# Kernel tuning notes

Measured on AMD Instinct MI355X. Metric: run time of the kernel, lower is better.

The kernel has to match this reference:

```python
import jax, jax.numpy as jnp
import numpy as np

B, T, C = 128, 512, 512
EPS = 1e-5


def setup_inputs() -> dict:
    key = jax.random.key(0)
    ks = jax.random.split(key, 12)
    s_tri = 1.0 / np.sqrt(T)   # rough torch Linear init scale (per-row fan-in varies; fixed for simplicity)
    s_fc1 = 1.0 / np.sqrt(C)
    s_fc2 = 1.0 / np.sqrt(2 * C)
    return {
        "inputs": jax.random.normal(ks[0], (B, T, C), dtype=jnp.float32),
        "ln1_w": jnp.ones((T, C), jnp.float32),
        "ln1_b": jnp.zeros((T, C), jnp.float32),
        "ln2_w": jnp.ones((T, C), jnp.float32),
        "ln2_b": jnp.zeros((T, C), jnp.float32),
        # Row s of triu_W corresponds to nn.Linear(s+1, 1); entries j> s are masked in reference().
        "triu_W": jax.random.uniform(ks[1], (T, T), jnp.float32, -s_tri, s_tri),
        "triu_b": jax.random.uniform(ks[2], (T,), jnp.float32, -s_tri, s_tri),
        "fc1_W": jax.random.uniform(ks[3], (2 * C, C), jnp.float32, -s_fc1, s_fc1),
        "fc1_b": jax.random.uniform(ks[4], (2 * C,), jnp.float32, -s_fc1, s_fc1),
        "fc2_W": jax.random.uniform(ks[5], (C, 2 * C), jnp.float32, -s_fc2, s_fc2),
        "fc2_b": jax.random.uniform(ks[6], (C,), jnp.float32, -s_fc2, s_fc2),
    }


def _layernorm_2d(x, w, b):
    # torch nn.LayerNorm((T, C)): normalize jointly over the last TWO dims.
    mu = jnp.mean(x, axis=(-2, -1), keepdims=True)
    var = jnp.var(x, axis=(-2, -1), keepdims=True)
    return (x - mu) * jax.lax.rsqrt(var + EPS) * w + b


def reference(inputs, ln1_w, ln1_b, ln2_w, ln2_b, triu_W, triu_b, fc1_W, fc1_b, fc2_W, fc2_b):
    x = _layernorm_2d(inputs, ln1_w, ln1_b)                       # [B,T,C]
    # TriU time mixer on x.mT ([B,C,T]): out[..., s] = sum_{t<=s} W[s,t]*x[..., t] + b[s]
    Wm = jnp.tril(triu_W)                                          # causal mask
    xm = jnp.einsum('btc,st->bsc', x, Wm) + triu_b[None, :, None]  # [B,T,C] (already back-transposed)
    x2 = _layernorm_2d(xm + inputs, ln2_w, ln2_b)                  # [B,T,C]
    h = jax.nn.gelu(jnp.einsum('btc,hc->bth', x2, fc1_W) + fc1_b, approximate=False)
    y = jnp.einsum('bth,ch->btc', h, fc2_W) + fc2_b
    return x2 + y
```

## Files before the change

### kernel.cpp

```cpp
#include <hip/hip_runtime.h>
#include <cstdint>

typedef unsigned short u16;
typedef __attribute__((ext_vector_type(8))) short s16x8;
typedef __attribute__((ext_vector_type(4))) float f32x4;
typedef __attribute__((ext_vector_type(8))) unsigned short u16x8;
typedef __attribute__((ext_vector_type(4))) unsigned short u16x4;

#define B_ 128
#define T_ 512
#define C_ 512
#define TC 262144

static __device__ __forceinline__ float bf2f(u16 u) {
  union { unsigned int i; float f; } v; v.i = ((unsigned int)u) << 16; return v.f;
}
static __device__ __forceinline__ u16 f2bf(float f) {
  union { float fv; unsigned int i; } v; v.fv = f;
  unsigned int r = (v.i + 0x7FFFu + ((v.i >> 16) & 1u)) >> 16;
  return (u16)r;
}

static __device__ __forceinline__ float gelu_fast(float x) {
  float x2 = x * x;
  float arg = 1.5957691216057308f * x * fmaf(0.044715f, x2, 1.0f);
  return x / (1.0f + __expf(-arg));
}

#define GLD16(gp, lp) __builtin_amdgcn_global_load_lds( \
    (const __attribute__((address_space(1))) void*)(gp), \
    (__attribute__((address_space(3))) void*)(lp), 16, 0, 0)


__global__ __launch_bounds__(256)
void reduce_stats_kernel(const float* __restrict__ X, float2* __restrict__ partials) {
  const int b = blockIdx.y, blk = blockIdx.x, tid = threadIdx.x;
  const float* p = X + (size_t)b * TC + (size_t)blk * 2048 + (size_t)tid * 8;
  f32x4 v0 = *(const f32x4*)p;
  f32x4 v1 = *(const f32x4*)(p + 4);
  float s = 0.f, q = 0.f;
#pragma unroll
  for (int i = 0; i < 4; ++i) { s += v0[i] + v1[i]; q += v0[i] * v0[i] + v1[i] * v1[i]; }
  for (int o = 32; o; o >>= 1) { s += __shfl_down(s, o); q += __shfl_down(q, o); }
  __shared__ float ss[4], qq[4];
  if ((tid & 63) == 0) { ss[tid >> 6] = s; qq[tid >> 6] = q; }
  __syncthreads();
  if (tid == 0)
    partials[(size_t)b * 128 + blk] =
        make_float2(ss[0] + ss[1] + ss[2] + ss[3], qq[0] + qq[1] + qq[2] + qq[3]);
}

__global__ __launch_bounds__(128)
void finalize_stats_kernel(const float2* __restrict__ partials, float2* __restrict__ stats) {
  const int b = blockIdx.x, tid = threadIdx.x;
  float2 v = partials[(size_t)b * 128 + tid];
  float s = v.x, q = v.y;
  for (int o = 32; o; o >>= 1) { s += __shfl_down(s, o); q += __shfl_down(q, o); }
  __shared__ float ss[2], qq[2];
  if ((tid & 63) == 0) { ss[tid >> 6] = s; qq[tid >> 6] = q; }
  __syncthreads();
  if (tid == 0) {
    float sm = ss[0] + ss[1], sq = qq[0] + qq[1];
    float mean = sm * (1.f / (float)TC);
    float var = sq * (1.f / (float)TC) - mean * mean;
    stats[b] = make_float2(mean, rsqrtf(var + 1e-5f));
  }
}

__global__ __launch_bounds__(64)
void finalize_stats4_kernel(const float2* __restrict__ partials, float2* __restrict__ stats) {
  const int b = blockIdx.x, tid = threadIdx.x;
  float s = 0.f, q = 0.f;
  if (tid < 4) { float2 v = partials[(size_t)b * 4 + tid]; s = v.x; q = v.y; }
  for (int o = 2; o; o >>= 1) { s += __shfl_down(s, o); q += __shfl_down(q, o); }
  if (tid == 0) {
    float mean = s * (1.f / (float)TC);
    float var = q * (1.f / (float)TC) - mean * mean;
    stats[b] = make_float2(mean, rsqrtf(var + 1e-5f));
  }
}


__global__ __launch_bounds__(256)
void ln1_transpose_kernel(const float* __restrict__ X, const float* __restrict__ W,
                          const float* __restrict__ Bv, const float2* __restrict__ stats,
                          u16* __restrict__ xT) {
  const int b = blockIdx.z;
  const int t0 = blockIdx.y * 64, c0 = blockIdx.x * 64;
  const float2 st = stats[b];
  const float mu = st.x, rs = st.y;
  __shared__ u16 tile[64][72];
  const int tid = threadIdx.x;
  const int rr = tid >> 4;
  const int cc = (tid & 15) * 4;
#pragma unroll
  for (int i = 0; i < 4; ++i) {
    const int lt = i * 16 + rr;
    const size_t wi = (size_t)(t0 + lt) * C_ + c0 + cc;
    f32x4 x = *(const f32x4*)(X + (size_t)b * TC + wi);
    f32x4 w = *(const f32x4*)(W + wi);
    f32x4 bb = *(const f32x4*)(Bv + wi);
#pragma unroll
    for (int j = 0; j < 4; ++j)
      tile[lt][cc + j] = f2bf((x[j] - mu) * rs * w[j] + bb[j]);
  }
  __syncthreads();
  const int c = tid >> 2;
  const int tg = (tid & 3) * 16;
  u16 buf[16];
#pragma unroll
  for (int i = 0; i < 16; ++i) buf[i] = tile[tg + i][c];
  const size_t o = (size_t)b * TC + (size_t)(c0 + c) * T_ + t0 + tg;
  u16x8 o0, o1;
#pragma unroll
  for (int i = 0; i < 8; ++i) { o0[i] = buf[i]; o1[i] = buf[8 + i]; }
  *(u16x8*)(xT + o) = o0;
  *(u16x8*)(xT + o + 8) = o1;
}


__global__ __launch_bounds__(256)
void ln2_apply_kernel(const u16* __restrict__ S, const float* __restrict__ W,
                      const float* __restrict__ Bv, const float2* __restrict__ stats,
                      u16* __restrict__ x2) {
  const size_t i = ((size_t)blockIdx.x * 256 + threadIdx.x) * 8;
  const int b = (int)(i >> 18);
  const size_t r = i & (size_t)(TC - 1);
  const float2 st = stats[b];
  const float mu = st.x, rs = st.y;
  u16x8 sv = *(const u16x8*)(S + i);
  f32x4 w0 = *(const f32x4*)(W + r);
  f32x4 w1 = *(const f32x4*)(W + r + 4);
  f32x4 b0 = *(const f32x4*)(Bv + r);
  f32x4 b1 = *(const f32x4*)(Bv + r + 4);
  u16x8 o;
#pragma unroll
  for (int j = 0; j < 4; ++j) {
    o[j]     = f2bf((bf2f(sv[j])     - mu) * rs * w0[j] + b0[j]);
    o[4 + j] = f2bf((bf2f(sv[4 + j]) - mu) * rs * w1[j] + b1[j]);
  }
  *(u16x8*)(x2 + i) = o;
}


__global__ __launch_bounds__(256)
void cvt_bf16_kernel(const float* __restrict__ X, u16* __restrict__ Y) {
  const size_t i = ((size_t)blockIdx.x * 256 + threadIdx.x) * 4;
  f32x4 v = *(const f32x4*)(X + i);
  u16x4 o;
#pragma unroll
  for (int j = 0; j < 4; ++j) o[j] = f2bf(v[j]);
  *(u16x4*)(Y + i) = o;
}

__global__ __launch_bounds__(256)
void tril_bf16_kernel(const float* __restrict__ Wt, u16* __restrict__ Y) {
  const int i = blockIdx.x * 256 + threadIdx.x;
  const int s = i >> 9, t = i & 511;
  Y[i] = f2bf(t <= s ? Wt[i] : 0.f);
}


template <int MODE>
__global__ __launch_bounds__(512, 2)
void gemm_bt_kernel(const u16* __restrict__ A, const u16* __restrict__ Bm,
                    int K, int lda, int ldb,
                    void* __restrict__ Cp, int ldc,
                    const float* __restrict__ bias,
                    const void* __restrict__ res,
                    long long strideB, long long strideC,
                    float2* __restrict__ stat_part) {
  __shared__ u16 As[2][256 * 64];
  __shared__ u16 Bs[2][256 * 64];
  const int tid = threadIdx.x;

  const int nwg = gridDim.x;
  const int orig = blockIdx.x;
  const int swz = (orig & 7) * (nwg >> 3) + (orig >> 3);
  int bx, by, bz;
  if (MODE == 0) { bz = swz >> 2; by = (swz >> 1) & 1; bx = swz & 1; }
  else if (MODE == 1) { bz = 0; by = swz >> 2; bx = swz & 3; }
  else { bz = 0; by = swz >> 1; bx = swz & 1; }

  const u16* Bp = Bm + (size_t)bz * (size_t)strideB;
  const int m0 = by * 256, n0 = bx * 256;
  int kTiles = K >> 6;
  if (MODE == 0) { const int need = (by + 1) * 4; if (need < kTiles) kTiles = need; }

  const int lane = tid & 63;
  const int wave = tid >> 6;
  const int wm = (wave >> 2) * 128;
  const int wn = (wave & 3) * 64;
  const int lr = lane & 15;
  const int kg = lane >> 4;

  f32x4 acc[8][4];
  const f32x4 zero = {0.f, 0.f, 0.f, 0.f};
#pragma unroll
  for (int m = 0; m < 8; ++m)
#pragma unroll
    for (int n = 0; n < 4; ++n) acc[m][n] = zero;

  auto STAGE = [&](int buf, int kt) {
    const int k0 = kt << 6;
#pragma unroll
    for (int p = 0; p < 4; ++p) {
      const int q = p * 512 + tid;
      const int r = q >> 3;
      const int kcs = (q & 7) ^ (r & 7);
      GLD16(A + (size_t)(m0 + r) * lda + k0 + (kcs << 3), &As[buf][q * 8]);
    }
#pragma unroll
    for (int p = 0; p < 4; ++p) {
      const int q = p * 512 + tid;
      const int r = q >> 3;
      const int kcs = (q & 7) ^ (r & 7);
      GLD16(Bp + (size_t)(n0 + r) * ldb + k0 + (kcs << 3), &Bs[buf][q * 8]);
    }
  };

  STAGE(0, 0);
  int cur = 0;
  for (int kt = 0; kt < kTiles; ++kt) {
    __syncthreads();
    if (kt + 1 < kTiles) STAGE(cur ^ 1, kt + 1);
#pragma unroll
    for (int kk = 0; kk < 2; ++kk) {
      s16x8 af[8], bf4[4];
#pragma unroll
      for (int m = 0; m < 8; ++m) {
        const int row = wm + m * 16 + lr;
        const int ch = (kk * 4 + kg) ^ (row & 7);
        af[m] = *(const s16x8*)&As[cur][row * 64 + ch * 8];
      }
#pragma unroll
      for (int n = 0; n < 4; ++n) {
        const int row = wn + n * 16 + lr;
        const int ch = (kk * 4 + kg) ^ (row & 7);
        bf4[n] = *(const s16x8*)&Bs[cur][row * 64 + ch * 8];
      }
#pragma unroll
      for (int m = 0; m < 8; ++m)
#pragma unroll
        for (int n = 0; n < 4; ++n)
          acc[m][n] = __builtin_amdgcn_mfma_f32_16x16x32_bf16(af[m], bf4[n], acc[m][n], 0, 0, 0);
    }
    cur ^= 1;
  }

  if (MODE == 0) {
    u16* Cptr = (u16*)Cp + (size_t)bz * (size_t)strideC;
    const float* inp = (const float*)res + (size_t)bz * (size_t)strideC;
    float psum = 0.f, psq = 0.f;
#pragma unroll
    for (int m = 0; m < 8; ++m) {
      const int rb = m0 + wm + m * 16 + kg * 4;
#pragma unroll
      for (int n = 0; n < 4; ++n) {
        const int col = n0 + wn + n * 16 + lr;
#pragma unroll
        for (int j = 0; j < 4; ++j) {
          const size_t idx = (size_t)(rb + j) * ldc + col;
          float v = acc[m][n][j] + inp[idx] + bias[rb + j];
          psum += v; psq += v * v;
          Cptr[idx] = f2bf(v);
        }
      }
    }
    for (int o = 32; o; o >>= 1) { psum += __shfl_down(psum, o); psq += __shfl_down(psq, o); }
    __shared__ float rs_[8], rq_[8];
    if (lane == 0) { rs_[wave] = psum; rq_[wave] = psq; }
    __syncthreads();
    if (tid == 0) {
      float s = 0.f, q = 0.f;
#pragma unroll
      for (int w = 0; w < 8; ++w) { s += rs_[w]; q += rq_[w]; }
      stat_part[(size_t)bz * 4 + by * 2 + bx] = make_float2(s, q);
    }
  } else if (MODE == 1) {
    u16* Cptr = (u16*)Cp;
#pragma unroll
    for (int m = 0; m < 8; ++m) {
      const int rb = m0 + wm + m * 16 + kg * 4;
#pragma unroll
      for (int n = 0; n < 4; ++n) {
        const int col = n0 + wn + n * 16 + lr;
        const float bs = bias[col];
#pragma unroll
        for (int j = 0; j < 4; ++j) {
          float v = acc[m][n][j] + bs;
          Cptr[(size_t)(rb + j) * ldc + col] = f2bf(gelu_fast(v));
        }
      }
    }
  } else {
    float* Cptr = (float*)Cp;
    const u16* x2p = (const u16*)res;
#pragma unroll
    for (int m = 0; m < 8; ++m) {
      const int rb = m0 + wm + m * 16 + kg * 4;
#pragma unroll
      for (int n = 0; n < 4; ++n) {
        const int col = n0 + wn + n * 16 + lr;
        const float bs = bias[col];
#pragma unroll
        for (int j = 0; j < 4; ++j) {
          const size_t idx = (size_t)(rb + j) * ldc + col;
          Cptr[idx] = acc[m][n][j] + bs + bf2f(x2p[idx]);
        }
      }
    }
  }
}


extern "C" void kernel_launch(void* const* d_in, const int* in_sizes, int n_in,
                              void* d_out, int out_size, void* d_ws, size_t ws_size,
                              hipStream_t stream) {
  const float* inputs = (const float*)d_in[0];
  const float* ln1_w  = (const float*)d_in[1];
  const float* ln1_b  = (const float*)d_in[2];
  const float* ln2_w  = (const float*)d_in[3];
  const float* ln2_b  = (const float*)d_in[4];
  const float* triu_W = (const float*)d_in[5];
  const float* triu_b = (const float*)d_in[6];
  const float* fc1_W  = (const float*)d_in[7];
  const float* fc1_b  = (const float*)d_in[8];
  const float* fc2_W  = (const float*)d_in[9];
  const float* fc2_b  = (const float*)d_in[10];
  float* out = (float*)d_out;
  (void)in_sizes; (void)n_in; (void)out_size; (void)ws_size;

  char* ws = (char*)d_ws;
  size_t off = 0;
  auto carve = [&](size_t bytes) {
    char* p = ws + off;
    off += (bytes + 255) & ~(size_t)255;
    return p;
  };
  u16* s_bf = (u16*)carve((size_t)B_ * T_ * C_ * 2);
  u16* xT   = (u16*)carve((size_t)B_ * T_ * C_ * 2);
  u16* x2   = xT;
  u16* h    = (u16*)carve((size_t)B_ * T_ * 2 * C_ * 2);
  u16* wmb  = (u16*)carve((size_t)T_ * T_ * 2);
  u16* w1b  = (u16*)carve((size_t)2 * C_ * C_ * 2);
  u16* w2b  = (u16*)carve((size_t)C_ * 2 * C_ * 2);
  float2* partials  = (float2*)carve(128 * 128 * sizeof(float2));
  float2* partials2 = (float2*)carve(128 * 4 * sizeof(float2));
  float2* stats1 = (float2*)carve(128 * sizeof(float2));
  float2* stats2 = (float2*)carve(128 * sizeof(float2));

  reduce_stats_kernel<<<dim3(128, 128), 256, 0, stream>>>(inputs, partials);
  finalize_stats_kernel<<<128, 128, 0, stream>>>(partials, stats1);
  ln1_transpose_kernel<<<dim3(8, 8, 128), 256, 0, stream>>>(inputs, ln1_w, ln1_b, stats1, xT);
  tril_bf16_kernel<<<1024, 256, 0, stream>>>(triu_W, wmb);
  cvt_bf16_kernel<<<512, 256, 0, stream>>>(fc1_W, w1b);
  cvt_bf16_kernel<<<512, 256, 0, stream>>>(fc2_W, w2b);
  gemm_bt_kernel<0><<<512, 512, 0, stream>>>(
      wmb, xT, 512, 512, 512, s_bf, 512, triu_b, inputs, (long long)TC, (long long)TC, partials2);
  finalize_stats4_kernel<<<128, 64, 0, stream>>>(partials2, stats2);
  ln2_apply_kernel<<<16384, 256, 0, stream>>>(s_bf, ln2_w, ln2_b, stats2, x2);
  gemm_bt_kernel<1><<<1024, 512, 0, stream>>>(
      x2, w1b, 512, 512, 512, h, 1024, fc1_b, nullptr, 0, 0, nullptr);
  gemm_bt_kernel<2><<<512, 512, 0, stream>>>(
      h, w2b, 1024, 1024, 1024, out, 512, fc2_b, x2, 0, 0, nullptr);
}
```

Baseline: 404.5 us.

## Stage GEMM epilogues through swizzled LDS for coalesced vector global stores

All three GEMM epilogue modes now write accumulator fragments into the shared-memory buffer (XOR-swizzled to avoid bank conflicts), then re-read it row-wise so each thread issues wide 16-byte global loads and stores. Before, each lane wrote scattered 2- or 4-byte elements with strided residual reads. The aim is to cut uncoalesced global traffic in the epilogue. The cost is extra LDS round trips and barriers, and MODE 0 now rounds the accumulator to bf16 before adding the residual and bias, which slightly changes its numerics.

```diff
diff --git a/kernel.cpp b/kernel.cpp
--- a/kernel.cpp
+++ b/kernel.cpp
@@ -170,8 +170,10 @@
                     const void* __restrict__ res,
                     long long strideB, long long strideC,
                     float2* __restrict__ stat_part) {
-  __shared__ u16 As[2][256 * 64];
-  __shared__ u16 Bs[2][256 * 64];
+  __shared__ u16 smem[65536];
+  __shared__ float rs_[8], rq_[8];
+  u16* Asb = smem;
+  u16* Bsb = smem + 32768;
   const int tid = threadIdx.x;
 
   const int nwg = gridDim.x;
@@ -208,14 +210,14 @@
       const int q = p * 512 + tid;
       const int r = q >> 3;
       const int kcs = (q & 7) ^ (r & 7);
-      GLD16(A + (size_t)(m0 + r) * lda + k0 + (kcs << 3), &As[buf][q * 8]);
+      GLD16(A + (size_t)(m0 + r) * lda + k0 + (kcs << 3), &Asb[buf * 16384 + q * 8]);
     }
 #pragma unroll
     for (int p = 0; p < 4; ++p) {
       const int q = p * 512 + tid;
       const int r = q >> 3;
       const int kcs = (q & 7) ^ (r & 7);
-      GLD16(Bp + (size_t)(n0 + r) * ldb + k0 + (kcs << 3), &Bs[buf][q * 8]);
+      GLD16(Bp + (size_t)(n0 + r) * ldb + k0 + (kcs << 3), &Bsb[buf * 16384 + q * 8]);
     }
   };
 
@@ -231,13 +233,13 @@
       for (int m = 0; m < 8; ++m) {
         const int row = wm + m * 16 + lr;
         const int ch = (kk * 4 + kg) ^ (row & 7);
-        af[m] = *(const s16x8*)&As[cur][row * 64 + ch * 8];
+        af[m] = *(const s16x8*)&Asb[cur * 16384 + row * 64 + ch * 8];
       }
 #pragma unroll
       for (int n = 0; n < 4; ++n) {
         const int row = wn + n * 16 + lr;
         const int ch = (kk * 4 + kg) ^ (row & 7);
-        bf4[n] = *(const s16x8*)&Bs[cur][row * 64 + ch * 8];
+        bf4[n] = *(const s16x8*)&Bsb[cur * 16384 + row * 64 + ch * 8];
       }
 #pragma unroll
       for (int m = 0; m < 8; ++m)
@@ -247,28 +249,50 @@
     }
     cur ^= 1;
   }
+
+  __syncthreads();
+  char* ep = (char*)smem;
 
   if (MODE == 0) {
     u16* Cptr = (u16*)Cp + (size_t)bz * (size_t)strideC;
     const float* inp = (const float*)res + (size_t)bz * (size_t)strideC;
+#pragma unroll
+    for (int m = 0; m < 8; ++m)
+#pragma unroll
+      for (int n = 0; n < 4; ++n) {
+        const int col = wn + n * 16 + lr;
+#pragma unroll
+        for (int j = 0; j < 4; ++j) {
+          const int row = wm + m * 16 + kg * 4 + j;
+          const int byt = row * 512 + ((((col >> 3) ^ (row & 31)) << 4)) + (col & 7) * 2;
+          *(u16*)(ep + byt) = f2bf(acc[m][n][j]);
+        }
+      }
+    __syncthreads();
+    const int frow = tid >> 1;
+    const int fhalf = tid & 1;
+    const int grow = m0 + frow;
+    const float bs = bias[grow];
+    u16* Crow = Cptr + (size_t)grow * ldc + n0 + fhalf * 128;
+    const float* irow = inp + (size_t)grow * ldc + n0 + fhalf * 128;
     float psum = 0.f, psq = 0.f;
 #pragma unroll
-    for (int m = 0; m < 8; ++m) {
-      const int rb = m0 + wm + m * 16 + kg * 4;
-#pragma unroll
-      for (int n = 0; n < 4; ++n) {
-        const int col = n0 + wn + n * 16 + lr;
-#pragma unroll
-        for (int j = 0; j < 4; ++j) {
-          const size_t idx = (size_t)(rb + j) * ldc + col;
-          float v = acc[m][n][j] + inp[idx] + bias[rb + j];
-          psum += v; psq += v * v;
-          Cptr[idx] = f2bf(v);
-        }
-      }
-    }
-    for (int o = 32; o; o >>= 1) { psum += __shfl_down(psum, o); psq += __shfl_down(psq, o); }
-    __shared__ float rs_[8], rq_[8];
+    for (int c16 = 0; c16 < 16; ++c16) {
+      const int c = fhalf * 16 + c16;
+      u16x8 e = *(const u16x8*)(ep + frow * 512 + ((c ^ (frow & 31)) << 4));
+      f32x4 i0 = *(const f32x4*)(irow + c16 * 8);
+      f32x4 i1 = *(const f32x4*)(irow + c16 * 8 + 4);
+      u16x8 o;
+#pragma unroll
+      for (int k = 0; k < 4; ++k) {
+        float v0 = bf2f(e[k]) + i0[k] + bs;
+        float v1 = bf2f(e[4 + k]) + i1[k] + bs;
+        psum += v0 + v1; psq += v0 * v0 + v1 * v1;
+        o[k] = f2bf(v0); o[4 + k] = f2bf(v1);
+      }
+      *(u16x8*)(Crow + c16 * 8) = o;
+    }
+    for (int sh = 32; sh; sh >>= 1) { psum += __shfl_down(psum, sh); psq += __shfl_down(psq, sh); }
     if (lane == 0) { rs_[wave] = psum; rq_[wave] = psq; }
     __syncthreads();
     if (tid == 0) {
@@ -280,35 +304,67 @@
   } else if (MODE == 1) {
     u16* Cptr = (u16*)Cp;
 #pragma unroll
-    for (int m = 0; m < 8; ++m) {
-      const int rb = m0 + wm + m * 16 + kg * 4;
+    for (int m = 0; m < 8; ++m)
 #pragma unroll
       for (int n = 0; n < 4; ++n) {
-        const int col = n0 + wn + n * 16 + lr;
-        const float bs = bias[col];
+        const int coll = wn + n * 16 + lr;
+        const float bsn = bias[n0 + coll];
 #pragma unroll
         for (int j = 0; j < 4; ++j) {
-          float v = acc[m][n][j] + bs;
-          Cptr[(size_t)(rb + j) * ldc + col] = f2bf(gelu_fast(v));
+          const int row = wm + m * 16 + kg * 4 + j;
+          const int byt = row * 512 + ((((coll >> 3) ^ (row & 31)) << 4)) + (coll & 7) * 2;
+          *(u16*)(ep + byt) = f2bf(gelu_fast(acc[m][n][j] + bsn));
         }
       }
+    __syncthreads();
+    const int frow = tid >> 1;
+    const int fhalf = tid & 1;
+    const int grow = m0 + frow;
+    u16* Crow = Cptr + (size_t)grow * ldc + n0 + fhalf * 128;
+#pragma unroll
+    for (int c16 = 0; c16 < 16; ++c16) {
+      const int c = fhalf * 16 + c16;
+      u16x8 e = *(const u16x8*)(ep + frow * 512 + ((c ^ (frow & 31)) << 4));
+      *(u16x8*)(Crow + c16 * 8) = e;
     }
   } else {
     float* Cptr = (float*)Cp;
     const u16* x2p = (const u16*)res;
 #pragma unroll
-    for (int m = 0; m < 8; ++m) {
-      const int rb = m0 + wm + m * 16 + kg * 4;
-#pragma unroll
-      for (int n = 0; n < 4; ++n) {
-        const int col = n0 + wn + n * 16 + lr;
-        const float bs = bias[col];
-#pragma unroll
-        for (int j = 0; j < 4; ++j) {
-          const size_t idx = (size_t)(rb + j) * ldc + col;
-          Cptr[idx] = acc[m][n][j] + bs + bf2f(x2p[idx]);
-        }
-      }
+    for (int half = 0; half < 2; ++half) {
+      if ((wave >> 2) == half) {
+#pragma unroll
+        for (int m = 0; m < 8; ++m)
+#pragma unroll
+          for (int n = 0; n < 4; ++n) {
+            const int coll = wn + n * 16 + lr;
+#pragma unroll
+            for (int j = 0; j < 4; ++j) {
+              const int lrow = m * 16 + kg * 4 + j;
+              const int byt = lrow * 1024 + ((((coll >> 2) ^ (lrow & 63)) << 4)) + (coll & 3) * 4;
+              *(float*)(ep + byt) = acc[m][n][j];
+            }
+          }
+      }
+      __syncthreads();
+      const int frow = tid >> 2;
+      const int seg = tid & 3;
+      const int grow = m0 + half * 128 + frow;
+      float* Crow = Cptr + (size_t)grow * ldc + n0;
+      const u16* xrow = x2p + (size_t)grow * ldc + n0;
+#pragma unroll
+      for (int c4 = 0; c4 < 16; ++c4) {
+        const int c = seg * 16 + c4;
+        f32x4 a = *(const f32x4*)(ep + frow * 1024 + ((c ^ (frow & 63)) << 4));
+        const int col0 = c * 4;
+        f32x4 bv = *(const f32x4*)(bias + n0 + col0);
+        u16x4 xv = *(const u16x4*)(xrow + col0);
+        f32x4 o;
+#pragma unroll
+        for (int k = 0; k < 4; ++k) o[k] = a[k] + bv[k] + bf2f(xv[k]);
+        *(f32x4*)(Crow + col0) = o;
+      }
+      __syncthreads();
     }
   }
 }
```

New measurement: 473.5 us. 17.0% more time.

## Split GEMM K-loop into four phased MFMA blocks with staggered A/B prefetch

Applied to the files above, without the earlier changes.

Restructures the GEMM main loop so each 64-wide K tile runs in four sub-phases. Each phase loads part of the A/B fragments from LDS, waits on lgkmcnt, then issues a block of MFMAs at raised wave priority. The A and B global-to-LDS loads are issued separately at different points, with A prefetched two tiles ahead, and explicit vmcnt waits and sched_barriers replace plain __syncthreads. The goal is to overlap LDS reads, global loads and MFMA work and to cut register pressure from the fragments. In exchange it adds extra barriers per tile and depends on fragile manual waitcnt counting.

```diff
diff --git a/kernel.cpp b/kernel.cpp
--- a/kernel.cpp
+++ b/kernel.cpp
@@ -170,8 +170,9 @@
                     const void* __restrict__ res,
                     long long strideB, long long strideC,
                     float2* __restrict__ stat_part) {
-  __shared__ u16 As[2][256 * 64];
-  __shared__ u16 Bs[2][256 * 64];
+  __shared__ u16 Asb[2 * 16384];
+  __shared__ u16 Bsb[2 * 16384];
+  __shared__ float rs_[8], rq_[8];
   const int tid = threadIdx.x;
 
   const int nwg = gridDim.x;
@@ -201,51 +202,116 @@
 #pragma unroll
     for (int n = 0; n < 4; ++n) acc[m][n] = zero;
 
-  auto STAGE = [&](int buf, int kt) {
-    const int k0 = kt << 6;
+  auto STAGE_A = [&](int t) {
+    const int k0 = t << 6;
+    const int d = (t & 1) * 16384;
 #pragma unroll
     for (int p = 0; p < 4; ++p) {
       const int q = p * 512 + tid;
       const int r = q >> 3;
       const int kcs = (q & 7) ^ (r & 7);
-      GLD16(A + (size_t)(m0 + r) * lda + k0 + (kcs << 3), &As[buf][q * 8]);
-    }
+      GLD16(A + (size_t)(m0 + r) * lda + k0 + (kcs << 3), &Asb[d + q * 8]);
+    }
+  };
+  auto STAGE_B = [&](int t) {
+    const int k0 = t << 6;
+    const int d = (t & 1) * 16384;
 #pragma unroll
     for (int p = 0; p < 4; ++p) {
       const int q = p * 512 + tid;
       const int r = q >> 3;
       const int kcs = (q & 7) ^ (r & 7);
-      GLD16(Bp + (size_t)(n0 + r) * ldb + k0 + (kcs << 3), &Bs[buf][q * 8]);
+      GLD16(Bp + (size_t)(n0 + r) * ldb + k0 + (kcs << 3), &Bsb[d + q * 8]);
     }
   };
 
-  STAGE(0, 0);
-  int cur = 0;
+  STAGE_A(0); STAGE_B(0); STAGE_A(1);
+
+  s16x8 af[8], bfv[2];
   for (int kt = 0; kt < kTiles; ++kt) {
-    __syncthreads();
-    if (kt + 1 < kTiles) STAGE(cur ^ 1, kt + 1);
-#pragma unroll
-    for (int kk = 0; kk < 2; ++kk) {
-      s16x8 af[8], bf4[4];
-#pragma unroll
-      for (int m = 0; m < 8; ++m) {
-        const int row = wm + m * 16 + lr;
-        const int ch = (kk * 4 + kg) ^ (row & 7);
-        af[m] = *(const s16x8*)&As[cur][row * 64 + ch * 8];
-      }
-#pragma unroll
-      for (int n = 0; n < 4; ++n) {
-        const int row = wn + n * 16 + lr;
-        const int ch = (kk * 4 + kg) ^ (row & 7);
-        bf4[n] = *(const s16x8*)&Bs[cur][row * 64 + ch * 8];
-      }
-#pragma unroll
-      for (int m = 0; m < 8; ++m)
-#pragma unroll
-        for (int n = 0; n < 4; ++n)
-          acc[m][n] = __builtin_amdgcn_mfma_f32_16x16x32_bf16(af[m], bf4[n], acc[m][n], 0, 0, 0);
-    }
-    cur ^= 1;
+    const int d = (kt & 1) * 16384;
+
+    if (kt + 1 < kTiles) asm volatile("s_waitcnt vmcnt(4)" ::: "memory");
+    else                 asm volatile("s_waitcnt vmcnt(0)" ::: "memory");
+    __builtin_amdgcn_s_barrier();
+    __builtin_amdgcn_sched_barrier(0);
+#pragma unroll
+    for (int m = 0; m < 8; ++m) {
+      const int row = wm + m * 16 + lr;
+      af[m] = *(const s16x8*)&Asb[d + row * 64 + ((kg ^ (row & 7)) << 3)];
+    }
+#pragma unroll
+    for (int n = 0; n < 2; ++n) {
+      const int row = wn + n * 16 + lr;
+      bfv[n] = *(const s16x8*)&Bsb[d + row * 64 + ((kg ^ (row & 7)) << 3)];
+    }
+    if (kt + 1 < kTiles) STAGE_B(kt + 1);
+    asm volatile("s_waitcnt lgkmcnt(0)" ::: "memory");
+    __builtin_amdgcn_sched_barrier(0);
+    __builtin_amdgcn_s_setprio(1);
+#pragma unroll
+    for (int m = 0; m < 8; ++m) {
+      acc[m][0] = __builtin_amdgcn_mfma_f32_16x16x32_bf16(af[m], bfv[0], acc[m][0], 0, 0, 0);
+      acc[m][1] = __builtin_amdgcn_mfma_f32_16x16x32_bf16(af[m], bfv[1], acc[m][1], 0, 0, 0);
+    }
+    __builtin_amdgcn_s_setprio(0);
+
+    __builtin_amdgcn_s_barrier();
+    __builtin_amdgcn_sched_barrier(0);
+#pragma unroll
+    for (int n = 0; n < 2; ++n) {
+      const int row = wn + (n + 2) * 16 + lr;
+      bfv[n] = *(const s16x8*)&Bsb[d + row * 64 + ((kg ^ (row & 7)) << 3)];
+    }
+    asm volatile("s_waitcnt lgkmcnt(0)" ::: "memory");
+    __builtin_amdgcn_sched_barrier(0);
+    __builtin_amdgcn_s_setprio(1);
+#pragma unroll
+    for (int m = 0; m < 8; ++m) {
+      acc[m][2] = __builtin_amdgcn_mfma_f32_16x16x32_bf16(af[m], bfv[0], acc[m][2], 0, 0, 0);
+      acc[m][3] = __builtin_amdgcn_mfma_f32_16x16x32_bf16(af[m], bfv[1], acc[m][3], 0, 0, 0);
+    }
+    __builtin_amdgcn_s_setprio(0);
+
+    __builtin_amdgcn_s_barrier();
+    __builtin_amdgcn_sched_barrier(0);
+#pragma unroll
+    for (int m = 0; m < 8; ++m) {
+      const int row = wm + m * 16 + lr;
+      af[m] = *(const s16x8*)&Asb[d + row * 64 + (((4 + kg) ^ (row & 7)) << 3)];
+    }
+#pragma unroll
+    for (int n = 0; n < 2; ++n) {
+      const int row = wn + n * 16 + lr;
+      bfv[n] = *(const s16x8*)&Bsb[d + row * 64 + (((4 + kg) ^ (row & 7)) << 3)];
+    }
+    asm volatile("s_waitcnt lgkmcnt(0)" ::: "memory");
+    __builtin_amdgcn_sched_barrier(0);
+    __builtin_amdgcn_s_setprio(1);
+#pragma unroll
+    for (int m = 0; m < 8; ++m) {
+      acc[m][0] = __builtin_amdgcn_mfma_f32_16x16x32_bf16(af[m], bfv[0], acc[m][0], 0, 0, 0);
+      acc[m][1] = __builtin_amdgcn_mfma_f32_16x16x32_bf16(af[m], bfv[1], acc[m][1], 0, 0, 0);
+    }
+    __builtin_amdgcn_s_setprio(0);
+
+    __builtin_amdgcn_s_barrier();
+    __builtin_amdgcn_sched_barrier(0);
+#pragma unroll
+    for (int n = 0; n < 2; ++n) {
+      const int row = wn + (n + 2) * 16 + lr;
+      bfv[n] = *(const s16x8*)&Bsb[d + row * 64 + (((4 + kg) ^ (row & 7)) << 3)];
+    }
+    if (kt + 2 < kTiles) STAGE_A(kt + 2);
+    asm volatile("s_waitcnt lgkmcnt(0)" ::: "memory");
+    __builtin_amdgcn_sched_barrier(0);
+    __builtin_amdgcn_s_setprio(1);
+#pragma unroll
+    for (int m = 0; m < 8; ++m) {
+      acc[m][2] = __builtin_amdgcn_mfma_f32_16x16x32_bf16(af[m], bfv[0], acc[m][2], 0, 0, 0);
+      acc[m][3] = __builtin_amdgcn_mfma_f32_16x16x32_bf16(af[m], bfv[1], acc[m][3], 0, 0, 0);
+    }
+    __builtin_amdgcn_s_setprio(0);
   }
 
   if (MODE == 0) {
@@ -268,7 +334,6 @@
       }
     }
     for (int o = 32; o; o >>= 1) { psum += __shfl_down(psum, o); psq += __shfl_down(psq, o); }
-    __shared__ float rs_[8], rq_[8];
     if (lane == 0) { rs_[wave] = psum; rq_[wave] = psq; }
     __syncthreads();
     if (tid == 0) {
```

New measurement: 382.5 us. 1.06x faster.

## Split A/B staging into finer-grained pipeline with manual waitcnt and priority hints

Applied to the files above, without the earlier changes.

Restructures the GEMM main loop so the A and B tiles are staged separately. A is prefetched two tiles ahead and B one tile ahead, with explicit vmcnt/lgkmcnt waits and raw barriers replacing __syncthreads. All A fragments and half of the B fragments are loaded up front, and MFMA blocks are wrapped in s_setprio to favour compute waves. Launch bounds drop to one block per SM-equivalent, and the shared stat arrays are hoisted. The deeper overlap is meant to hide global-load latency, at the cost of more registers, fragile hand-counted vmcnt values and possibly lower occupancy.

```diff
diff --git a/kernel.cpp b/kernel.cpp
--- a/kernel.cpp
+++ b/kernel.cpp
@@ -162,7 +162,7 @@
 
 
 template <int MODE>
-__global__ __launch_bounds__(512, 2)
+__global__ __launch_bounds__(512, 1)
 void gemm_bt_kernel(const u16* __restrict__ A, const u16* __restrict__ Bm,
                     int K, int lda, int ldb,
                     void* __restrict__ Cp, int ldc,
@@ -170,8 +170,9 @@
                     const void* __restrict__ res,
                     long long strideB, long long strideC,
                     float2* __restrict__ stat_part) {
-  __shared__ u16 As[2][256 * 64];
-  __shared__ u16 Bs[2][256 * 64];
+  __shared__ u16 Asb[2 * 16384];
+  __shared__ u16 Bsb[2 * 16384];
+  __shared__ float rs_[8], rq_[8];
   const int tid = threadIdx.x;
 
   const int nwg = gridDim.x;
@@ -201,51 +202,79 @@
 #pragma unroll
     for (int n = 0; n < 4; ++n) acc[m][n] = zero;
 
-  auto STAGE = [&](int buf, int kt) {
-    const int k0 = kt << 6;
+  auto STAGE_A = [&](int t) {
+    const int k0 = t << 6;
+    const int d = (t & 1) * 16384;
 #pragma unroll
     for (int p = 0; p < 4; ++p) {
       const int q = p * 512 + tid;
       const int r = q >> 3;
       const int kcs = (q & 7) ^ (r & 7);
-      GLD16(A + (size_t)(m0 + r) * lda + k0 + (kcs << 3), &As[buf][q * 8]);
-    }
+      GLD16(A + (size_t)(m0 + r) * lda + k0 + (kcs << 3), &Asb[d + q * 8]);
+    }
+  };
+  auto STAGE_B = [&](int t) {
+    const int k0 = t << 6;
+    const int d = (t & 1) * 16384;
 #pragma unroll
     for (int p = 0; p < 4; ++p) {
       const int q = p * 512 + tid;
       const int r = q >> 3;
       const int kcs = (q & 7) ^ (r & 7);
-      GLD16(Bp + (size_t)(n0 + r) * ldb + k0 + (kcs << 3), &Bs[buf][q * 8]);
+      GLD16(Bp + (size_t)(n0 + r) * ldb + k0 + (kcs << 3), &Bsb[d + q * 8]);
     }
   };
 
-  STAGE(0, 0);
-  int cur = 0;
+  STAGE_A(0); STAGE_B(0); STAGE_A(1);
+
   for (int kt = 0; kt < kTiles; ++kt) {
-    __syncthreads();
-    if (kt + 1 < kTiles) STAGE(cur ^ 1, kt + 1);
-#pragma unroll
-    for (int kk = 0; kk < 2; ++kk) {
-      s16x8 af[8], bf4[4];
-#pragma unroll
-      for (int m = 0; m < 8; ++m) {
-        const int row = wm + m * 16 + lr;
-        const int ch = (kk * 4 + kg) ^ (row & 7);
-        af[m] = *(const s16x8*)&As[cur][row * 64 + ch * 8];
-      }
-#pragma unroll
-      for (int n = 0; n < 4; ++n) {
-        const int row = wn + n * 16 + lr;
-        const int ch = (kk * 4 + kg) ^ (row & 7);
-        bf4[n] = *(const s16x8*)&Bs[cur][row * 64 + ch * 8];
-      }
-#pragma unroll
-      for (int m = 0; m < 8; ++m)
-#pragma unroll
-        for (int n = 0; n < 4; ++n)
-          acc[m][n] = __builtin_amdgcn_mfma_f32_16x16x32_bf16(af[m], bf4[n], acc[m][n], 0, 0, 0);
-    }
-    cur ^= 1;
+    const int d = (kt & 1) * 16384;
+
+    if (kt + 1 < kTiles) asm volatile("s_waitcnt vmcnt(4)" ::: "memory");
+    else                 asm volatile("s_waitcnt vmcnt(0)" ::: "memory");
+    __builtin_amdgcn_s_barrier();
+    asm volatile("" ::: "memory");
+
+    s16x8 a0[8], a1[8], b0[4], b1[4];
+#pragma unroll
+    for (int m = 0; m < 8; ++m) {
+      const int row = wm + m * 16 + lr;
+      const u16* base = &Asb[d + row * 64];
+      a0[m] = *(const s16x8*)(base + (((kg)     ^ (row & 7)) << 3));
+      a1[m] = *(const s16x8*)(base + (((4 + kg) ^ (row & 7)) << 3));
+    }
+#pragma unroll
+    for (int n = 0; n < 4; ++n) {
+      const int row = wn + n * 16 + lr;
+      b0[n] = *(const s16x8*)(&Bsb[d + row * 64] + (((kg) ^ (row & 7)) << 3));
+    }
+    if (kt + 1 < kTiles) STAGE_B(kt + 1);
+
+    __builtin_amdgcn_s_setprio(1);
+#pragma unroll
+    for (int m = 0; m < 8; ++m)
+#pragma unroll
+      for (int n = 0; n < 4; ++n)
+        acc[m][n] = __builtin_amdgcn_mfma_f32_16x16x32_bf16(a0[m], b0[n], acc[m][n], 0, 0, 0);
+    __builtin_amdgcn_s_setprio(0);
+
+#pragma unroll
+    for (int n = 0; n < 4; ++n) {
+      const int row = wn + n * 16 + lr;
+      b1[n] = *(const s16x8*)(&Bsb[d + row * 64] + (((4 + kg) ^ (row & 7)) << 3));
+    }
+    asm volatile("s_waitcnt lgkmcnt(0)" ::: "memory");
+    __builtin_amdgcn_s_barrier();
+    asm volatile("" ::: "memory");
+    if (kt + 2 < kTiles) STAGE_A(kt + 2);
+
+    __builtin_amdgcn_s_setprio(1);
+#pragma unroll
+    for (int m = 0; m < 8; ++m)
+#pragma unroll
+      for (int n = 0; n < 4; ++n)
+        acc[m][n] = __builtin_amdgcn_mfma_f32_16x16x32_bf16(a1[m], b1[n], acc[m][n], 0, 0, 0);
+    __builtin_amdgcn_s_setprio(0);
   }
 
   if (MODE == 0) {
@@ -268,7 +297,6 @@
       }
     }
     for (int o = 32; o; o >>= 1) { psum += __shfl_down(psum, o); psq += __shfl_down(psq, o); }
-    __shared__ float rs_[8], rq_[8];
     if (lane == 0) { rs_[wave] = psum; rq_[wave] = psq; }
     __syncthreads();
     if (tid == 0) {
```

After: 373.3 us. 7.7% less time.
